# Performance work log

Hardware: AMD Instinct MI355X
Metric: run time of the kernel (lower is better)

## Reference

```python
import jax, jax.numpy as jnp
import numpy as np

N = 16384   # points (batch=1, divisible by patch_size so padding is identity)
C = 512     # channels
H = 8       # num_heads
K = 1024    # patch_size
G = 48      # voxel grid extent
EPS = 1e-5
SCALE = (C // H) ** -0.5


def setup_inputs() -> dict:
    rng = np.random.default_rng(0)
    # unique occupied voxels
    flat = rng.choice(G ** 3, size=N, replace=False)
    gx = flat // (G * G); gy = (flat // G) % G; gz = flat % G
    coords = np.stack([gx, gy, gz], 1).astype(np.int64)
    # occupancy LUT on padded grid -> neighbor index per 3x3x3 kernel offset (-1 = empty)
    lut = -np.ones(((G + 2) ** 3,), np.int64)
    def flt(c):
        return ((c[:, 0] + 1) * (G + 2) + (c[:, 1] + 1)) * (G + 2) + (c[:, 2] + 1)
    lut[flt(coords)] = np.arange(N)
    offs = np.array([[dx, dy, dz] for dx in (-1, 0, 1) for dy in (-1, 0, 1) for dz in (-1, 0, 1)], np.int64)
    nbr = np.stack([lut[flt(coords + o)] for o in offs], 1)  # [N,27]
    # Morton (z-order) serialization order
    def spread(v):
        v = v.astype(np.int64); r = np.zeros_like(v)
        for b in range(6):
            r |= ((v >> b) & 1) << (3 * b)
        return r
    code = (spread(gx) << 2) | (spread(gy) << 1) | spread(gz)
    order = np.argsort(code, kind='stable').astype(np.int32)

    key = jax.random.key(0)
    ks = jax.random.split(key, 8)
    s = 0.02
    p = lambda k, shape: jax.random.normal(k, shape, jnp.float32) * s
    return dict(
        feat=jax.random.normal(ks[0], (N, C), jnp.float32),
        neighbor_idx=jnp.asarray(nbr, jnp.int32),
        order=jnp.asarray(order, jnp.int32),
        cpe_w=p(ks[1], (27, C, C)), cpe_b=jnp.zeros((C,), jnp.float32),
        cpe_lin_w=p(ks[2], (C, C)), cpe_lin_b=jnp.zeros((C,), jnp.float32),
        cpe_ln_g=jnp.ones((C,), jnp.float32), cpe_ln_b=jnp.zeros((C,), jnp.float32),
        ln1_g=jnp.ones((C,), jnp.float32), ln1_b=jnp.zeros((C,), jnp.float32),
        qkv_w=p(ks[3], (3 * C, C)), qkv_b=jnp.zeros((3 * C,), jnp.float32),
        proj_w=p(ks[4], (C, C)), proj_b=jnp.zeros((C,), jnp.float32),
        ln2_g=jnp.ones((C,), jnp.float32), ln2_b=jnp.zeros((C,), jnp.float32),
        fc1_w=p(ks[5], (4 * C, C)), fc1_b=jnp.zeros((4 * C,), jnp.float32),
        fc2_w=p(ks[6], (C, 4 * C)), fc2_b=jnp.zeros((C,), jnp.float32),
    )


def _ln(x, g, b):
    m = x.mean(-1, keepdims=True)
    v = ((x - m) ** 2).mean(-1, keepdims=True)
    return (x - m) * jax.lax.rsqrt(v + EPS) * g + b


def _block(feat, neighbor_idx, order, cpe_w, cpe_b, cpe_lin_w, cpe_lin_b,
           cpe_ln_g, cpe_ln_b, ln1_g, ln1_b, qkv_w, qkv_b, proj_w, proj_b,
           ln2_g, ln2_b, fc1_w, fc1_b, fc2_w, fc2_b):
    # ---- CPE: SubMConv3d(3x3x3) -> Linear -> LayerNorm, residual ----
    valid = neighbor_idx >= 0
    idx = jnp.maximum(neighbor_idx, 0)
    h = jnp.zeros_like(feat)
    for kk in range(27):  # fixed kernel volume
        g = jnp.where(valid[:, kk:kk + 1], feat[idx[:, kk]], 0.0)
        h = h + g @ cpe_w[kk].T
    h = h + cpe_b
    h = h @ cpe_lin_w.T + cpe_lin_b
    h = _ln(h, cpe_ln_g, cpe_ln_b)
    feat = feat + h
    # ---- Serialized windowed attention (pre-norm, residual) ----
    x = _ln(feat, ln1_g, ln1_b)
    qkv = (x @ qkv_w.T + qkv_b)[order]                 # gather by serialized order
    qkv = qkv.reshape(N // K, K, 3, H, C // H)         # [P,K,3,H,hd]
    q = qkv[:, :, 0].transpose(0, 2, 1, 3)             # [P,H,K,hd]
    k = qkv[:, :, 1].transpose(0, 2, 1, 3)
    v = qkv[:, :, 2].transpose(0, 2, 1, 3)
    attn = jax.nn.softmax(jnp.einsum('phkd,phjd->phkj', q * SCALE, k), axis=-1)
    o = jnp.einsum('phkj,phjd->phkd', attn, v).transpose(0, 2, 1, 3).reshape(N, C)
    inverse = jnp.argsort(order)                       # scatter back
    o = o[inverse] @ proj_w.T + proj_b
    feat = feat + o
    # ---- MLP (pre-norm, residual) ----
    x = _ln(feat, ln2_g, ln2_b)
    x = jax.nn.gelu(x @ fc1_w.T + fc1_b, approximate=False)
    x = x @ fc2_w.T + fc2_b
    return feat + x


def reference(feat, neighbor_idx, order, cpe_w, cpe_b, cpe_lin_w, cpe_lin_b,
              cpe_ln_g, cpe_ln_b, ln1_g, ln1_b, qkv_w, qkv_b, proj_w, proj_b,
              ln2_g, ln2_b, fc1_w, fc1_b, fc2_w, fc2_b):
    return _block(feat, neighbor_idx, order, cpe_w, cpe_b, cpe_lin_w, cpe_lin_b,
                  cpe_ln_g, cpe_ln_b, ln1_g, ln1_b, qkv_w, qkv_b, proj_w, proj_b,
                  ln2_g, ln2_b, fc1_w, fc1_b, fc2_w, fc2_b)
```

## Files before the change

### kernel.cpp

```cpp
#include <hip/hip_runtime.h>
#include <math.h>

typedef unsigned short u16;
typedef unsigned int u32;
typedef __attribute__((ext_vector_type(8))) short short8;
typedef __attribute__((ext_vector_type(4))) float f32x4;

#define NPTS 16384

__device__ __forceinline__ u16 f2bf(float f) {
  u32 u = __float_as_uint(f);
  u = (u + 0x7fffu + ((u >> 16) & 1u)) >> 16;
  return (u16)u;
}
__device__ __forceinline__ float bf2f(u16 u) {
  return __uint_as_float((u32)u << 16);
}

__device__ __forceinline__ void gl2lds16(const u16* g, u16* l) {
  __builtin_amdgcn_global_load_lds(
      (const __attribute__((address_space(1))) u32*)g,
      (__attribute__((address_space(3))) u32*)l, 16, 0, 0);
}

__device__ __forceinline__ float wredsum(float v) {
#pragma unroll
  for (int m = 1; m < 64; m <<= 1) v += __shfl_xor(v, m, 64);
  return v;
}

__global__ void cvt_all(const float* __restrict__ w0, const float* __restrict__ w1,
                        const float* __restrict__ w2, const float* __restrict__ w3,
                        const float* __restrict__ w4, const float* __restrict__ w5,
                        u16* __restrict__ dst) {
  const int i = blockIdx.x * 256 + threadIdx.x;
  const float* s;
  int li;
  if (i < 1769472) { s = w0; li = i; }
  else if (i < 1835008) { s = w1; li = i - 1769472; }
  else if (i < 2031616) { s = w2; li = i - 1835008; }
  else if (i < 2097152) { s = w3; li = i - 2031616; }
  else if (i < 2359296) { s = w4; li = i - 2097152; }
  else { s = w5; li = i - 2359296; }
  float4 v = ((const float4*)s)[li];
  ushort4 o;
  o.x = f2bf(v.x); o.y = f2bf(v.y); o.z = f2bf(v.z); o.w = f2bf(v.w);
  ((ushort4*)dst)[i] = o;
}

__global__ void cvt_feat(const float* __restrict__ s, u16* __restrict__ d) {
  int i = blockIdx.x * 256 + threadIdx.x;
  if (i >= (NPTS + 1) * 128) return;
  ushort4 o;
  if (i < NPTS * 128) {
    float4 v = ((const float4*)s)[i];
    o.x = f2bf(v.x); o.y = f2bf(v.y); o.z = f2bf(v.z); o.w = f2bf(v.w);
  } else {
    o.x = 0; o.y = 0; o.z = 0; o.w = 0;
  }
  ((ushort4*)d)[i] = o;
}

__global__ void mkinv(const int* __restrict__ order, int* __restrict__ inv) {
  int i = blockIdx.x * 256 + threadIdx.x;
  if (i < NPTS) inv[order[i]] = i;
}

__global__ void reduce3b(const u16* __restrict__ part, const float* __restrict__ bias,
                         u16* __restrict__ o) {
  const int i = blockIdx.x * 256 + threadIdx.x;
  const ushort4* p4 = (const ushort4*)part;
  const ushort4 a = p4[i];
  const ushort4 b = p4[i + 2097152];
  const ushort4 c = p4[i + 4194304];
  const float4 bb = ((const float4*)bias)[i & 127];
  ushort4 r;
  r.x = f2bf(bf2f(a.x) + bf2f(b.x) + bf2f(c.x) + bb.x);
  r.y = f2bf(bf2f(a.y) + bf2f(b.y) + bf2f(c.y) + bb.y);
  r.z = f2bf(bf2f(a.z) + bf2f(b.z) + bf2f(c.z) + bb.z);
  r.w = f2bf(bf2f(a.w) + bf2f(b.w) + bf2f(c.w) + bb.w);
  ((ushort4*)o)[i] = r;
}

__global__ __launch_bounds__(256) void vtrans(const u16* __restrict__ vr,
                                              u16* __restrict__ vt) {
  __shared__ u16 t[64 * 72];
  const int bid = blockIdx.x;
  const int ph = bid >> 4, jt = bid & 15;
  const u16* src = vr + (size_t)ph * 65536 + jt * 64 * 64;
  u16* dst = vt + (size_t)ph * 65536 + jt * 64;
  const int tid = threadIdx.x;
  {
    const int j = tid >> 2, d0 = (tid & 3) * 16;
    uint4 w0 = *(const uint4*)(src + j * 64 + d0);
    uint4 w1 = *(const uint4*)(src + j * 64 + d0 + 8);
    *(uint4*)&t[j * 72 + d0] = w0;
    *(uint4*)&t[j * 72 + d0 + 8] = w1;
  }
  __syncthreads();
  {
    const int dr = tid >> 2, j0 = (tid & 3) * 16;
    u16 tmp[16];
#pragma unroll
    for (int e = 0; e < 16; e++) tmp[e] = t[(j0 + e) * 72 + dr];
    *(uint4*)(dst + (size_t)dr * 1024 + j0) = *(uint4*)&tmp[0];
    *(uint4*)(dst + (size_t)dr * 1024 + j0 + 8) = *(uint4*)&tmp[8];
  }
}

__global__ __launch_bounds__(256, 2) void gemm_cpe(
    const u16* __restrict__ Abase, const u16* __restrict__ Bw,
    const int* __restrict__ nbr, u16* __restrict__ part) {
  __shared__ __align__(16) u16 sA[128 * 32];
  __shared__ __align__(16) u16 sB[128 * 32];
  const int tid = threadIdx.x;
  const int wave = tid >> 6, lane = tid & 63;
  const int quad = lane >> 4, tl = lane & 15;
  const int wr = wave >> 1, wc = wave & 1;
  const int m0 = blockIdx.x * 128, n0 = blockIdx.y * 128;
  const int kk0 = blockIdx.z * 9;
  const int srow = lane >> 2, scol = lane & 3;

  int r[2]; int ca[2]; size_t brow[2];
#pragma unroll
  for (int o = 0; o < 2; o++) {
    r[o] = wave * 32 + o * 16 + srow;
    const int sw = (r[o] + (r[o] >> 2)) & 3;
    ca[o] = (scol ^ sw) * 8;
    brow[o] = (size_t)(n0 + r[o]) * 512 + ca[o];
  }
  u16* ldsA0 = &sA[(wave * 32) * 32];
  u16* ldsA1 = &sA[(wave * 32 + 16) * 32];
  u16* ldsB0 = &sB[(wave * 32) * 32];
  u16* ldsB1 = &sB[(wave * 32 + 16) * 32];

  f32x4 acc[4][4] = {};
  int nxt0 = nbr[(m0 + r[0]) * 27 + kk0];
  int nxt1 = nbr[(m0 + r[1]) * 27 + kk0];

  for (int s = 0; s < 9; s++) {
    const int kk = kk0 + s;
    const int g0 = nxt0 < 0 ? NPTS : nxt0;
    const int g1 = nxt1 < 0 ? NPTS : nxt1;
    if (s < 8) {
      nxt0 = nbr[(m0 + r[0]) * 27 + kk + 1];
      nxt1 = nbr[(m0 + r[1]) * 27 + kk + 1];
    }
    const u16* a0 = Abase + (size_t)g0 * 512 + ca[0];
    const u16* a1 = Abase + (size_t)g1 * 512 + ca[1];
    const u16* b0 = Bw + (size_t)kk * 262144 + brow[0];
    const u16* b1 = Bw + (size_t)kk * 262144 + brow[1];
#pragma unroll 1
    for (int kc = 0; kc < 512; kc += 32) {
      __syncthreads();
      gl2lds16(a0 + kc, ldsA0);
      gl2lds16(b0 + kc, ldsB0);
      gl2lds16(a1 + kc, ldsA1);
      gl2lds16(b1 + kc, ldsB1);
      __syncthreads();
      short8 fa[4], fb[4];
#pragma unroll
      for (int i = 0; i < 4; i++) {
        const int ra = wr * 64 + i * 16 + tl;
        fa[i] = *(const short8*)&sA[ra * 32 + ((quad ^ ((ra + (ra >> 2)) & 3)) * 8)];
        const int rb = wc * 64 + i * 16 + tl;
        fb[i] = *(const short8*)&sB[rb * 32 + ((quad ^ ((rb + (rb >> 2)) & 3)) * 8)];
      }
#pragma unroll
      for (int i = 0; i < 4; i++)
#pragma unroll
        for (int j = 0; j < 4; j++)
          acc[i][j] = __builtin_amdgcn_mfma_f32_16x16x32_bf16(fa[i], fb[j], acc[i][j], 0, 0, 0);
    }
  }

  u16* pz = part + (size_t)blockIdx.z * NPTS * 512;
#pragma unroll
  for (int i = 0; i < 4; i++) {
    const int mB = m0 + wr * 64 + i * 16 + quad * 4;
#pragma unroll
    for (int j = 0; j < 4; j++) {
      const int n = n0 + wc * 64 + j * 16 + tl;
      f32x4 c = acc[i][j];
#pragma unroll
      for (int rr = 0; rr < 4; rr++)
        pz[(size_t)(mB + rr) * 512 + n] = f2bf(c[rr]);
    }
  }
}

enum { EP_BF16 = 0, EP_QKV = 2, EP_RES = 3, EP_GELU = 4 };

template <int EP>
__global__ __launch_bounds__(256, 2) void gemm_nt(
    const u16* __restrict__ A, const u16* __restrict__ B, int M, int N, int K,
    const float* __restrict__ bias, float* __restrict__ outf,
    u16* __restrict__ outb, const float* __restrict__ res,
    const int* __restrict__ inv, u16* __restrict__ oq, u16* __restrict__ okk,
    u16* __restrict__ ov) {
  __shared__ __align__(16) u16 sA[128 * 32];
  __shared__ __align__(16) u16 sB[128 * 32];
  const int tid = threadIdx.x;
  const int wave = tid >> 6, lane = tid & 63;
  const int quad = lane >> 4, tl = lane & 15;
  const int wr = wave >> 1, wc = wave & 1;
  const int m0 = blockIdx.x * 128, n0 = blockIdx.y * 128;
  const int srow = lane >> 2, scol = lane & 3;

  f32x4 acc[4][4] = {};

  for (int kt = 0; kt < K; kt += 32) {
    __syncthreads();
#pragma unroll
    for (int o = 0; o < 2; o++) {
      const int r = wave * 32 + o * 16 + srow;
      const int sw = (r + (r >> 2)) & 3;
      const int ca = (scol ^ sw) * 8;
      gl2lds16(A + (size_t)(m0 + r) * K + kt + ca, &sA[(wave * 32 + o * 16) * 32]);
      gl2lds16(B + (size_t)(n0 + r) * K + kt + ca, &sB[(wave * 32 + o * 16) * 32]);
    }
    __syncthreads();
    short8 fa[4], fb[4];
#pragma unroll
    for (int i = 0; i < 4; i++) {
      const int ra = wr * 64 + i * 16 + tl;
      fa[i] = *(const short8*)&sA[ra * 32 + ((quad ^ ((ra + (ra >> 2)) & 3)) * 8)];
      const int rb = wc * 64 + i * 16 + tl;
      fb[i] = *(const short8*)&sB[rb * 32 + ((quad ^ ((rb + (rb >> 2)) & 3)) * 8)];
    }
#pragma unroll
    for (int i = 0; i < 4; i++)
#pragma unroll
      for (int j = 0; j < 4; j++)
        acc[i][j] = __builtin_amdgcn_mfma_f32_16x16x32_bf16(fa[i], fb[j], acc[i][j], 0, 0, 0);
  }

#pragma unroll
  for (int i = 0; i < 4; i++) {
    const int mB = m0 + wr * 64 + i * 16 + quad * 4;
#pragma unroll
    for (int j = 0; j < 4; j++) {
      const int n = n0 + wc * 64 + j * 16 + tl;
      const float bv = bias[n];
      f32x4 c = acc[i][j];
#pragma unroll
      for (int r = 0; r < 4; r++) {
        const int m = mB + r;
        float v = c[r] + bv;
        if (EP == EP_BF16) {
          outb[(size_t)m * N + n] = f2bf(v);
        } else if (EP == EP_RES) {
          outf[(size_t)m * N + n] = v + res[(size_t)m * N + n];
        } else if (EP == EP_GELU) {
          float g = 0.5f * v * (1.0f + erff(v * 0.70710678118654752f));
          outb[(size_t)m * N + n] = f2bf(g);
        } else if (EP == EP_QKV) {
          const int s = n >> 9, hh = (n >> 6) & 7, d = n & 63;
          const int pos = inv[m];
          const size_t base = (size_t)((pos >> 10) * 8 + hh) * 65536;
          const int jj = pos & 1023;
          if (s == 0) oq[base + (size_t)jj * 64 + d] = f2bf(v * 0.125f);
          else if (s == 1) okk[base + (size_t)jj * 64 + d] = f2bf(v);
          else ov[base + (size_t)jj * 64 + d] = f2bf(v);
        }
      }
    }
  }
}

__global__ __launch_bounds__(256, 2) void attn(
    const u16* __restrict__ qs, const u16* __restrict__ kk_s,
    const u16* __restrict__ vts, const int* __restrict__ order,
    u16* __restrict__ obf) {
  __shared__ __align__(16) u16 Qt[128 * 64];
  __shared__ __align__(16) u16 Kt[64 * 64];
  __shared__ __align__(16) u16 Vt[64 * 64];
  __shared__ __align__(16) u16 Pl[4][32 * 72];
  const int tid = threadIdx.x;
  const int wave = tid >> 6, lane = tid & 63;
  const int quad = lane >> 4, tl = lane & 15;
  const int bid = blockIdx.x;
  const int p = bid >> 6, h = (bid >> 3) & 7, qt = bid & 7;
  const size_t base = (size_t)(p * 8 + h) * 65536;

  {
    const u16* Qg = qs + base + qt * 8192;
#pragma unroll
    for (int i = 0; i < 4; i++) {
      const int op = wave * 4 + i;
      const int r = op * 8 + (lane >> 3);
      const int c8 = ((lane & 7) ^ (r & 7)) * 8;
      gl2lds16(Qg + r * 64 + c8, &Qt[op * 512]);
    }
  }

  float ls[2][4] = {};
  f32x4 acco[2][4] = {};

  for (int kt = 0; kt < 16; kt++) {
    __syncthreads();
    const u16* Kg = kk_s + base + kt * 4096;
    const u16* Vg = vts + base + kt * 64;
#pragma unroll
    for (int i = 0; i < 2; i++) {
      const int op = wave * 2 + i;
      const int r = op * 8 + (lane >> 3);
      const int c8 = ((lane & 7) ^ (r & 7)) * 8;
      gl2lds16(Kg + r * 64 + c8, &Kt[op * 512]);
      gl2lds16(Vg + r * 1024 + c8, &Vt[op * 512]);
    }
    __syncthreads();

    f32x4 accs[2][4] = {};
#pragma unroll
    for (int kd = 0; kd < 2; kd++) {
      short8 qa[2], kb[4];
#pragma unroll
      for (int a = 0; a < 2; a++) {
        const int r = wave * 32 + a * 16 + tl;
        const int oct = (kd * 4 + quad) ^ (r & 7);
        qa[a] = *(const short8*)&Qt[r * 64 + oct * 8];
      }
#pragma unroll
      for (int b = 0; b < 4; b++) {
        const int r = b * 16 + tl;
        const int oct = (kd * 4 + quad) ^ (r & 7);
        kb[b] = *(const short8*)&Kt[r * 64 + oct * 8];
      }
#pragma unroll
      for (int a = 0; a < 2; a++)
#pragma unroll
        for (int b = 0; b < 4; b++)
          accs[a][b] = __builtin_amdgcn_mfma_f32_16x16x32_bf16(qa[a], kb[b], accs[a][b], 0, 0, 0);
    }

    u16* plw = &Pl[wave][0];
#pragma unroll
    for (int a = 0; a < 2; a++)
#pragma unroll
      for (int c = 0; c < 4; c++) {
#pragma unroll
        for (int r = 0; r < 4; r++) {
          const float pe = __expf(accs[a][c][r]);
          accs[a][c][r] = pe;
          ls[a][r] += pe;
          plw[(a * 16 + quad * 4 + r) * 72 + c * 16 + tl] = f2bf(pe);
        }
      }

#pragma unroll
    for (int k2 = 0; k2 < 2; k2++) {
      short8 pa[2], vb[4];
#pragma unroll
      for (int a = 0; a < 2; a++)
        pa[a] = *(const short8*)&plw[(a * 16 + tl) * 72 + k2 * 32 + quad * 8];
#pragma unroll
      for (int b = 0; b < 4; b++) {
        const int rb = b * 16 + tl;
        vb[b] = *(const short8*)&Vt[rb * 64 + (((k2 * 4 + quad) ^ (rb & 7)) * 8)];
      }
#pragma unroll
      for (int a = 0; a < 2; a++)
#pragma unroll
        for (int b = 0; b < 4; b++)
          acco[a][b] = __builtin_amdgcn_mfma_f32_16x16x32_bf16(pa[a], vb[b], acco[a][b], 0, 0, 0);
    }
  }

#pragma unroll
  for (int a = 0; a < 2; a++)
#pragma unroll
    for (int r = 0; r < 4; r++) {
#pragma unroll
      for (int mk = 1; mk < 16; mk <<= 1) ls[a][r] += __shfl_xor(ls[a][r], mk, 64);
    }

  const int q0 = p * 1024 + qt * 128 + wave * 32;
#pragma unroll
  for (int a = 0; a < 2; a++)
#pragma unroll
    for (int r = 0; r < 4; r++) {
      const int orig = order[q0 + a * 16 + quad * 4 + r];
      const float il = 1.0f / ls[a][r];
#pragma unroll
      for (int b = 0; b < 4; b++)
        obf[(size_t)orig * 512 + h * 64 + b * 16 + tl] = f2bf(acco[a][b][r] * il);
    }
}

__global__ __launch_bounds__(256, 4) void ln_fuse1(
    const u16* __restrict__ h2, const float* __restrict__ feat,
    const float* __restrict__ cg, const float* __restrict__ cb,
    const float* __restrict__ g1, const float* __restrict__ b1,
    float* __restrict__ feat1, u16* __restrict__ xbf) {
  const int wave = threadIdx.x >> 6, lane = threadIdx.x & 63;
  const size_t row = (size_t)blockIdx.x * 4 + wave;
  const int c0 = lane * 4, c1 = 256 + lane * 4;
  const u16* hr = h2 + row * 512;
  ushort4 ha = *(const ushort4*)(hr + c0);
  ushort4 hb = *(const ushort4*)(hr + c1);
  float h[8];
  h[0] = bf2f(ha.x); h[1] = bf2f(ha.y); h[2] = bf2f(ha.z); h[3] = bf2f(ha.w);
  h[4] = bf2f(hb.x); h[5] = bf2f(hb.y); h[6] = bf2f(hb.z); h[7] = bf2f(hb.w);
  float s = 0.0f, q = 0.0f;
#pragma unroll
  for (int i = 0; i < 8; i++) { s += h[i]; q += h[i] * h[i]; }
  s = wredsum(s); q = wredsum(q);
  const float mean = s * (1.0f / 512.0f);
  const float var = q * (1.0f / 512.0f) - mean * mean;
  const float rs = rsqrtf(var + 1e-5f);
  float4 ga = *(const float4*)(cg + c0), gb = *(const float4*)(cg + c1);
  float4 ba = *(const float4*)(cb + c0), bb = *(const float4*)(cb + c1);
  const float* fr = feat + row * 512;
  float4 fa = *(const float4*)(fr + c0), fb = *(const float4*)(fr + c1);
  float f[8];
  f[0] = fa.x + (h[0] - mean) * rs * ga.x + ba.x;
  f[1] = fa.y + (h[1] - mean) * rs * ga.y + ba.y;
  f[2] = fa.z + (h[2] - mean) * rs * ga.z + ba.z;
  f[3] = fa.w + (h[3] - mean) * rs * ga.w + ba.w;
  f[4] = fb.x + (h[4] - mean) * rs * gb.x + bb.x;
  f[5] = fb.y + (h[5] - mean) * rs * gb.y + bb.y;
  f[6] = fb.z + (h[6] - mean) * rs * gb.z + bb.z;
  f[7] = fb.w + (h[7] - mean) * rs * gb.w + bb.w;
  float* f1r = feat1 + row * 512;
  *(float4*)(f1r + c0) = make_float4(f[0], f[1], f[2], f[3]);
  *(float4*)(f1r + c1) = make_float4(f[4], f[5], f[6], f[7]);
  float s2 = 0.0f, q2 = 0.0f;
#pragma unroll
  for (int i = 0; i < 8; i++) { s2 += f[i]; q2 += f[i] * f[i]; }
  s2 = wredsum(s2); q2 = wredsum(q2);
  const float mean2 = s2 * (1.0f / 512.0f);
  const float var2 = q2 * (1.0f / 512.0f) - mean2 * mean2;
  const float rs2 = rsqrtf(var2 + 1e-5f);
  float4 g1a = *(const float4*)(g1 + c0), g1b = *(const float4*)(g1 + c1);
  float4 b1a = *(const float4*)(b1 + c0), b1b = *(const float4*)(b1 + c1);
  ushort4 o0, o1;
  o0.x = f2bf((f[0] - mean2) * rs2 * g1a.x + b1a.x);
  o0.y = f2bf((f[1] - mean2) * rs2 * g1a.y + b1a.y);
  o0.z = f2bf((f[2] - mean2) * rs2 * g1a.z + b1a.z);
  o0.w = f2bf((f[3] - mean2) * rs2 * g1a.w + b1a.w);
  o1.x = f2bf((f[4] - mean2) * rs2 * g1b.x + b1b.x);
  o1.y = f2bf((f[5] - mean2) * rs2 * g1b.y + b1b.y);
  o1.z = f2bf((f[6] - mean2) * rs2 * g1b.z + b1b.z);
  o1.w = f2bf((f[7] - mean2) * rs2 * g1b.w + b1b.w);
  *(ushort4*)(xbf + row * 512 + c0) = o0;
  *(ushort4*)(xbf + row * 512 + c1) = o1;
}

__global__ __launch_bounds__(256, 4) void ln_only(
    const float* __restrict__ x, const float* __restrict__ g,
    const float* __restrict__ b_, u16* __restrict__ o) {
  const int wave = threadIdx.x >> 6, lane = threadIdx.x & 63;
  const size_t row = (size_t)blockIdx.x * 4 + wave;
  const int c0 = lane * 4, c1 = 256 + lane * 4;
  const float* xr = x + row * 512;
  float4 a = *(const float4*)(xr + c0);
  float4 b = *(const float4*)(xr + c1);
  float s = a.x + a.y + a.z + a.w + b.x + b.y + b.z + b.w;
  float q = a.x * a.x + a.y * a.y + a.z * a.z + a.w * a.w +
            b.x * b.x + b.y * b.y + b.z * b.z + b.w * b.w;
  s = wredsum(s); q = wredsum(q);
  const float mean = s * (1.0f / 512.0f);
  const float var = q * (1.0f / 512.0f) - mean * mean;
  const float rs = rsqrtf(var + 1e-5f);
  float4 ga = *(const float4*)(g + c0), gb = *(const float4*)(g + c1);
  float4 ba = *(const float4*)(b_ + c0), bb = *(const float4*)(b_ + c1);
  ushort4 o0, o1;
  o0.x = f2bf((a.x - mean) * rs * ga.x + ba.x);
  o0.y = f2bf((a.y - mean) * rs * ga.y + ba.y);
  o0.z = f2bf((a.z - mean) * rs * ga.z + ba.z);
  o0.w = f2bf((a.w - mean) * rs * ga.w + ba.w);
  o1.x = f2bf((b.x - mean) * rs * gb.x + bb.x);
  o1.y = f2bf((b.y - mean) * rs * gb.y + bb.y);
  o1.z = f2bf((b.z - mean) * rs * gb.z + bb.z);
  o1.w = f2bf((b.w - mean) * rs * gb.w + bb.w);
  *(ushort4*)(o + row * 512 + c0) = o0;
  *(ushort4*)(o + row * 512 + c1) = o1;
}

extern "C" void kernel_launch(void* const* d_in, const int* in_sizes, int n_in,
                              void* d_out, int out_size, void* d_ws, size_t ws_size,
                              hipStream_t stream) {
  (void)in_sizes; (void)n_in; (void)out_size; (void)ws_size;
  const float* feat = (const float*)d_in[0];
  const int* nbr = (const int*)d_in[1];
  const int* order = (const int*)d_in[2];
  const float* cpe_w = (const float*)d_in[3];
  const float* cpe_b = (const float*)d_in[4];
  const float* cpe_lin_w = (const float*)d_in[5];
  const float* cpe_lin_b = (const float*)d_in[6];
  const float* cpe_ln_g = (const float*)d_in[7];
  const float* cpe_ln_b = (const float*)d_in[8];
  const float* ln1_g = (const float*)d_in[9];
  const float* ln1_b = (const float*)d_in[10];
  const float* qkv_w = (const float*)d_in[11];
  const float* qkv_b = (const float*)d_in[12];
  const float* proj_w = (const float*)d_in[13];
  const float* proj_b = (const float*)d_in[14];
  const float* ln2_g = (const float*)d_in[15];
  const float* ln2_b = (const float*)d_in[16];
  const float* fc1_w = (const float*)d_in[17];
  const float* fc1_b = (const float*)d_in[18];
  const float* fc2_w = (const float*)d_in[19];
  const float* fc2_b = (const float*)d_in[20];
  float* out = (float*)d_out;

  char* ws = (char*)d_ws;
  size_t off = 0;
  auto alloc = [&](size_t bytes) {
    char* p = ws + off;
    off += (bytes + 255) & ~(size_t)255;
    return p;
  };
  u16* featbf = (u16*)alloc((size_t)(NPTS + 1) * 512 * 2);
  u16* w_cpe = (u16*)alloc((size_t)27 * 512 * 512 * 2);
  u16* w_cl = (u16*)alloc((size_t)512 * 512 * 2);
  u16* w_qkv = (u16*)alloc((size_t)1536 * 512 * 2);
  u16* w_proj = (u16*)alloc((size_t)512 * 512 * 2);
  u16* w_fc1 = (u16*)alloc((size_t)2048 * 512 * 2);
  u16* w_fc2 = (u16*)alloc((size_t)512 * 2048 * 2);
  u16* hbf = (u16*)alloc((size_t)NPTS * 512 * 2);
  char* big = alloc((size_t)NPTS * 2048 * 2);
  float* feat1 = (float*)alloc((size_t)NPTS * 512 * 4);
  int* inv = (int*)alloc((size_t)NPTS * 4);

  u16* part = (u16*)big;
  u16* h2 = (u16*)big;
  u16* qsb = (u16*)big;
  u16* ksb = qsb + (size_t)NPTS * 512;
  u16* vrow = ksb + (size_t)NPTS * 512;
  u16* vtb = vrow + (size_t)NPTS * 512;
  u16* tbf = (u16*)big;
  u16* xbf = hbf;
  u16* obf = hbf;
  u16* x2bf = featbf;

  cvt_feat<<<dim3(((NPTS + 1) * 128 + 255) / 256), dim3(256), 0, stream>>>(feat, featbf);
  cvt_all<<<dim3(10240), dim3(256), 0, stream>>>(cpe_w, cpe_lin_w, qkv_w, proj_w,
                                                 fc1_w, fc2_w, w_cpe);
  mkinv<<<dim3(NPTS / 256), dim3(256), 0, stream>>>(order, inv);

  gemm_cpe<<<dim3(128, 4, 3), dim3(256), 0, stream>>>(featbf, w_cpe, nbr, part);
  reduce3b<<<dim3(8192), dim3(256), 0, stream>>>(part, cpe_b, hbf);
  gemm_nt<EP_BF16><<<dim3(128, 4), dim3(256), 0, stream>>>(
      hbf, w_cl, NPTS, 512, 512, cpe_lin_b, nullptr, h2, nullptr, nullptr,
      nullptr, nullptr, nullptr);
  ln_fuse1<<<dim3(NPTS / 4), dim3(256), 0, stream>>>(
      h2, feat, cpe_ln_g, cpe_ln_b, ln1_g, ln1_b, feat1, xbf);
  gemm_nt<EP_QKV><<<dim3(128, 12), dim3(256), 0, stream>>>(
      xbf, w_qkv, NPTS, 1536, 512, qkv_b, nullptr, nullptr, nullptr, inv,
      qsb, ksb, vrow);
  vtrans<<<dim3(2048), dim3(256), 0, stream>>>(vrow, vtb);
  attn<<<dim3(1024), dim3(256), 0, stream>>>(qsb, ksb, vtb, order, obf);
  gemm_nt<EP_RES><<<dim3(128, 4), dim3(256), 0, stream>>>(
      obf, w_proj, NPTS, 512, 512, proj_b, out, nullptr, feat1, nullptr,
      nullptr, nullptr, nullptr);
  ln_only<<<dim3(NPTS / 4), dim3(256), 0, stream>>>(out, ln2_g, ln2_b, x2bf);
  gemm_nt<EP_GELU><<<dim3(128, 16), dim3(256), 0, stream>>>(
      x2bf, w_fc1, NPTS, 2048, 512, fc1_b, nullptr, tbf, nullptr, nullptr,
      nullptr, nullptr, nullptr);
  gemm_nt<EP_RES><<<dim3(128, 4), dim3(256), 0, stream>>>(
      tbf, w_fc2, NPTS, 512, 2048, fc2_b, out, nullptr, out, nullptr,
      nullptr, nullptr, nullptr);
}
```

Measured before the change: 636.8 us.

## Replace dense 27-offset CPE GEMM with compacted sparse neighbor-pair GEMM

The sparse 3x3x3 conv used to multiply every point by all 27 offset weights, substituting a zero row for empty neighbors, and then summed three partial buffers. Now the valid (point, neighbor) pairs are counted, offset and scattered per kernel offset into compact 128-row tiles. A GEMM runs only over those tiles, and a per-point reduce sums the pair outputs and adds the bias. This removes the multiply work on empty neighbors, which is most of it at this grid occupancy, at the cost of three small bookkeeping kernels and an extra gather-reduce pass. A fixed MAXP buffer cap silently drops pairs if the inputs are denser than expected.

```diff
diff --git a/kernel.cpp b/kernel.cpp
--- a/kernel.cpp
+++ b/kernel.cpp
@@ -3,10 +3,13 @@
 
 typedef unsigned short u16;
 typedef unsigned int u32;
+typedef unsigned long long u64;
 typedef __attribute__((ext_vector_type(8))) short short8;
 typedef __attribute__((ext_vector_type(4))) float f32x4;
 
 #define NPTS 16384
+#define MAXP 98304
+#define MAXTILE 3483
 
 __device__ __forceinline__ u16 f2bf(float f) {
   u32 u = __float_as_uint(f);
@@ -24,6 +27,11 @@
 }
 
 __device__ __forceinline__ float wredsum(float v) {
+#pragma unroll
+  for (int m = 1; m < 64; m <<= 1) v += __shfl_xor(v, m, 64);
+  return v;
+}
+__device__ __forceinline__ int wredsumi(int v) {
 #pragma unroll
   for (int m = 1; m < 64; m <<= 1) v += __shfl_xor(v, m, 64);
   return v;
@@ -66,20 +74,173 @@
   if (i < NPTS) inv[order[i]] = i;
 }
 
-__global__ void reduce3b(const u16* __restrict__ part, const float* __restrict__ bias,
-                         u16* __restrict__ o) {
-  const int i = blockIdx.x * 256 + threadIdx.x;
-  const ushort4* p4 = (const ushort4*)part;
-  const ushort4 a = p4[i];
-  const ushort4 b = p4[i + 2097152];
-  const ushort4 c = p4[i + 4194304];
-  const float4 bb = ((const float4*)bias)[i & 127];
-  ushort4 r;
-  r.x = f2bf(bf2f(a.x) + bf2f(b.x) + bf2f(c.x) + bb.x);
-  r.y = f2bf(bf2f(a.y) + bf2f(b.y) + bf2f(c.y) + bb.y);
-  r.z = f2bf(bf2f(a.z) + bf2f(b.z) + bf2f(c.z) + bb.z);
-  r.w = f2bf(bf2f(a.w) + bf2f(b.w) + bf2f(c.w) + bb.w);
-  ((ushort4*)o)[i] = r;
+__global__ __launch_bounds__(256) void cpe_count(const int* __restrict__ nbr,
+                                                 int* __restrict__ cnt) {
+  __shared__ int wc[4];
+  const int kk = blockIdx.x;
+  int c = 0;
+  for (int i = threadIdx.x; i < NPTS; i += 256)
+    c += (nbr[i * 27 + kk] >= 0) ? 1 : 0;
+  c = wredsumi(c);
+  if ((threadIdx.x & 63) == 0) wc[threadIdx.x >> 6] = c;
+  __syncthreads();
+  if (threadIdx.x == 0) cnt[kk] = wc[0] + wc[1] + wc[2] + wc[3];
+}
+
+__global__ void cpe_off(const int* __restrict__ cnt, int* __restrict__ off,
+                        int* __restrict__ tkk, int* __restrict__ meta) {
+  if (threadIdx.x != 0 || blockIdx.x != 0) return;
+  int pos = 0, t = 0;
+  for (int kk = 0; kk < 27; kk++) {
+    off[kk] = pos;
+    int tk = (cnt[kk] + 127) >> 7;
+    if (pos + tk * 128 > MAXP) tk = (MAXP - pos) >> 7;
+    for (int u = 0; u < tk; u++) tkk[t + u] = kk;
+    t += tk;
+    pos += tk * 128;
+  }
+  meta[0] = t;
+}
+
+__global__ __launch_bounds__(256) void cpe_scatter(
+    const int* __restrict__ nbr, const int* __restrict__ cnt,
+    const int* __restrict__ off, int* __restrict__ pairj,
+    int* __restrict__ pairpos) {
+  __shared__ int wcnt[4];
+  __shared__ int running_s;
+  const int kk = blockIdx.x;
+  const int tid = threadIdx.x, wave = tid >> 6, lane = tid & 63;
+  const int base = off[kk];
+  if (tid == 0) running_s = 0;
+  __syncthreads();
+  for (int c0 = 0; c0 < NPTS; c0 += 256) {
+    const int i = c0 + tid;
+    const int v = nbr[i * 27 + kk];
+    const bool valid = v >= 0;
+    const u64 m = __ballot(valid);
+    if (lane == 0) wcnt[wave] = __popcll(m);
+    __syncthreads();
+    int woff = 0;
+    for (int w = 0; w < wave; w++) woff += wcnt[w];
+    const int ctot = wcnt[0] + wcnt[1] + wcnt[2] + wcnt[3];
+    const int rank = running_s + woff + __popcll(m & ((1ull << lane) - 1ull));
+    int pp = -1;
+    if (valid) {
+      const int t = base + rank;
+      if (t < MAXP) { pairj[t] = v; pp = t; }
+    }
+    pairpos[i * 27 + kk] = pp;
+    __syncthreads();
+    if (tid == 0) running_s += ctot;
+    __syncthreads();
+  }
+  const int total = cnt[kk];
+  const int padded = (total + 127) & ~127;
+  for (int p = total + tid; p < padded; p += 256)
+    if (base + p < MAXP) pairj[base + p] = NPTS;
+}
+
+__global__ __launch_bounds__(256, 2) void gemm_pair(
+    const u16* __restrict__ Abase, const u16* __restrict__ Bw,
+    const int* __restrict__ meta, const int* __restrict__ tkk,
+    const int* __restrict__ pairj, u16* __restrict__ outp) {
+  if ((int)blockIdx.x >= meta[0]) return;
+  __shared__ __align__(16) u16 sA[128 * 32];
+  __shared__ __align__(16) u16 sB[128 * 32];
+  const int tid = threadIdx.x;
+  const int wave = tid >> 6, lane = tid & 63;
+  const int quad = lane >> 4, tl = lane & 15;
+  const int wr = wave >> 1, wc = wave & 1;
+  const int p0 = blockIdx.x * 128, n0 = blockIdx.y * 128;
+  const int kk = tkk[blockIdx.x];
+  const int srow = lane >> 2, scol = lane & 3;
+
+  int r[2]; int ca[2];
+#pragma unroll
+  for (int o = 0; o < 2; o++) {
+    r[o] = wave * 32 + o * 16 + srow;
+    const int sw = (r[o] + (r[o] >> 2)) & 3;
+    ca[o] = (scol ^ sw) * 8;
+  }
+  const int j0 = pairj[p0 + r[0]];
+  const int j1 = pairj[p0 + r[1]];
+  const u16* a0 = Abase + (size_t)j0 * 512 + ca[0];
+  const u16* a1 = Abase + (size_t)j1 * 512 + ca[1];
+  const u16* b0 = Bw + (size_t)kk * 262144 + (size_t)(n0 + r[0]) * 512 + ca[0];
+  const u16* b1 = Bw + (size_t)kk * 262144 + (size_t)(n0 + r[1]) * 512 + ca[1];
+  u16* ldsA0 = &sA[(wave * 32) * 32];
+  u16* ldsA1 = &sA[(wave * 32 + 16) * 32];
+  u16* ldsB0 = &sB[(wave * 32) * 32];
+  u16* ldsB1 = &sB[(wave * 32 + 16) * 32];
+
+  f32x4 acc[4][4] = {};
+#pragma unroll 1
+  for (int kc = 0; kc < 512; kc += 32) {
+    __syncthreads();
+    gl2lds16(a0 + kc, ldsA0);
+    gl2lds16(b0 + kc, ldsB0);
+    gl2lds16(a1 + kc, ldsA1);
+    gl2lds16(b1 + kc, ldsB1);
+    __syncthreads();
+    short8 fa[4], fb[4];
+#pragma unroll
+    for (int i = 0; i < 4; i++) {
+      const int ra = wr * 64 + i * 16 + tl;
+      fa[i] = *(const short8*)&sA[ra * 32 + ((quad ^ ((ra + (ra >> 2)) & 3)) * 8)];
+      const int rb = wc * 64 + i * 16 + tl;
+      fb[i] = *(const short8*)&sB[rb * 32 + ((quad ^ ((rb + (rb >> 2)) & 3)) * 8)];
+    }
+#pragma unroll
+    for (int i = 0; i < 4; i++)
+#pragma unroll
+      for (int j = 0; j < 4; j++)
+        acc[i][j] = __builtin_amdgcn_mfma_f32_16x16x32_bf16(fa[i], fb[j], acc[i][j], 0, 0, 0);
+  }
+
+#pragma unroll
+  for (int i = 0; i < 4; i++) {
+    const int pB = p0 + wr * 64 + i * 16 + quad * 4;
+#pragma unroll
+    for (int j = 0; j < 4; j++) {
+      const int n = n0 + wc * 64 + j * 16 + tl;
+      f32x4 c = acc[i][j];
+#pragma unroll
+      for (int rr = 0; rr < 4; rr++)
+        outp[(size_t)(pB + rr) * 512 + n] = f2bf(c[rr]);
+    }
+  }
+}
+
+__global__ __launch_bounds__(256, 4) void cpe_reduce(
+    const u16* __restrict__ outp, const int* __restrict__ pairpos,
+    const float* __restrict__ bias, u16* __restrict__ h) {
+  const int wave = threadIdx.x >> 6, lane = threadIdx.x & 63;
+  const int i = blockIdx.x * 4 + wave;
+  const int c = lane * 8;
+  float acc[8];
+  const float4 b0 = *(const float4*)(bias + c);
+  const float4 b1 = *(const float4*)(bias + c + 4);
+  acc[0] = b0.x; acc[1] = b0.y; acc[2] = b0.z; acc[3] = b0.w;
+  acc[4] = b1.x; acc[5] = b1.y; acc[6] = b1.z; acc[7] = b1.w;
+  const int* pp = pairpos + i * 27;
+#pragma unroll 1
+  for (int kk = 0; kk < 27; kk++) {
+    const int pos = pp[kk];
+    if (pos >= 0) {
+      const u16* row = outp + (size_t)pos * 512 + c;
+      ushort4 u0 = *(const ushort4*)row;
+      ushort4 u1 = *(const ushort4*)(row + 4);
+      acc[0] += bf2f(u0.x); acc[1] += bf2f(u0.y);
+      acc[2] += bf2f(u0.z); acc[3] += bf2f(u0.w);
+      acc[4] += bf2f(u1.x); acc[5] += bf2f(u1.y);
+      acc[6] += bf2f(u1.z); acc[7] += bf2f(u1.w);
+    }
+  }
+  ushort4 o0, o1;
+  o0.x = f2bf(acc[0]); o0.y = f2bf(acc[1]); o0.z = f2bf(acc[2]); o0.w = f2bf(acc[3]);
+  o1.x = f2bf(acc[4]); o1.y = f2bf(acc[5]); o1.z = f2bf(acc[6]); o1.w = f2bf(acc[7]);
+  *(ushort4*)(h + (size_t)i * 512 + c) = o0;
+  *(ushort4*)(h + (size_t)i * 512 + c + 4) = o1;
 }
 
 __global__ __launch_bounds__(256) void vtrans(const u16* __restrict__ vr,
@@ -105,87 +266,6 @@
     for (int e = 0; e < 16; e++) tmp[e] = t[(j0 + e) * 72 + dr];
     *(uint4*)(dst + (size_t)dr * 1024 + j0) = *(uint4*)&tmp[0];
     *(uint4*)(dst + (size_t)dr * 1024 + j0 + 8) = *(uint4*)&tmp[8];
-  }
-}
-
-__global__ __launch_bounds__(256, 2) void gemm_cpe(
-    const u16* __restrict__ Abase, const u16* __restrict__ Bw,
-    const int* __restrict__ nbr, u16* __restrict__ part) {
-  __shared__ __align__(16) u16 sA[128 * 32];
-  __shared__ __align__(16) u16 sB[128 * 32];
-  const int tid = threadIdx.x;
-  const int wave = tid >> 6, lane = tid & 63;
-  const int quad = lane >> 4, tl = lane & 15;
-  const int wr = wave >> 1, wc = wave & 1;
-  const int m0 = blockIdx.x * 128, n0 = blockIdx.y * 128;
-  const int kk0 = blockIdx.z * 9;
-  const int srow = lane >> 2, scol = lane & 3;
-
-  int r[2]; int ca[2]; size_t brow[2];
-#pragma unroll
-  for (int o = 0; o < 2; o++) {
-    r[o] = wave * 32 + o * 16 + srow;
-    const int sw = (r[o] + (r[o] >> 2)) & 3;
-    ca[o] = (scol ^ sw) * 8;
-    brow[o] = (size_t)(n0 + r[o]) * 512 + ca[o];
-  }
-  u16* ldsA0 = &sA[(wave * 32) * 32];
-  u16* ldsA1 = &sA[(wave * 32 + 16) * 32];
-  u16* ldsB0 = &sB[(wave * 32) * 32];
-  u16* ldsB1 = &sB[(wave * 32 + 16) * 32];
-
-  f32x4 acc[4][4] = {};
-  int nxt0 = nbr[(m0 + r[0]) * 27 + kk0];
-  int nxt1 = nbr[(m0 + r[1]) * 27 + kk0];
-
-  for (int s = 0; s < 9; s++) {
-    const int kk = kk0 + s;
-    const int g0 = nxt0 < 0 ? NPTS : nxt0;
-    const int g1 = nxt1 < 0 ? NPTS : nxt1;
-    if (s < 8) {
-      nxt0 = nbr[(m0 + r[0]) * 27 + kk + 1];
-      nxt1 = nbr[(m0 + r[1]) * 27 + kk + 1];
-    }
-    const u16* a0 = Abase + (size_t)g0 * 512 + ca[0];
-    const u16* a1 = Abase + (size_t)g1 * 512 + ca[1];
-    const u16* b0 = Bw + (size_t)kk * 262144 + brow[0];
-    const u16* b1 = Bw + (size_t)kk * 262144 + brow[1];
-#pragma unroll 1
-    for (int kc = 0; kc < 512; kc += 32) {
-      __syncthreads();
-      gl2lds16(a0 + kc, ldsA0);
-      gl2lds16(b0 + kc, ldsB0);
-      gl2lds16(a1 + kc, ldsA1);
-      gl2lds16(b1 + kc, ldsB1);
-      __syncthreads();
-      short8 fa[4], fb[4];
-#pragma unroll
-      for (int i = 0; i < 4; i++) {
-        const int ra = wr * 64 + i * 16 + tl;
-        fa[i] = *(const short8*)&sA[ra * 32 + ((quad ^ ((ra + (ra >> 2)) & 3)) * 8)];
-        const int rb = wc * 64 + i * 16 + tl;
-        fb[i] = *(const short8*)&sB[rb * 32 + ((quad ^ ((rb + (rb >> 2)) & 3)) * 8)];
-      }
-#pragma unroll
-      for (int i = 0; i < 4; i++)
-#pragma unroll
-        for (int j = 0; j < 4; j++)
-          acc[i][j] = __builtin_amdgcn_mfma_f32_16x16x32_bf16(fa[i], fb[j], acc[i][j], 0, 0, 0);
-    }
-  }
-
-  u16* pz = part + (size_t)blockIdx.z * NPTS * 512;
-#pragma unroll
-  for (int i = 0; i < 4; i++) {
-    const int mB = m0 + wr * 64 + i * 16 + quad * 4;
-#pragma unroll
-    for (int j = 0; j < 4; j++) {
-      const int n = n0 + wc * 64 + j * 16 + tl;
-      f32x4 c = acc[i][j];
-#pragma unroll
-      for (int rr = 0; rr < 4; rr++)
-        pz[(size_t)(mB + rr) * 512 + n] = f2bf(c[rr]);
-    }
   }
 }
 
@@ -523,8 +603,14 @@
   char* big = alloc((size_t)NPTS * 2048 * 2);
   float* feat1 = (float*)alloc((size_t)NPTS * 512 * 4);
   int* inv = (int*)alloc((size_t)NPTS * 4);
-
-  u16* part = (u16*)big;
+  int* cnt = (int*)alloc(27 * 4);
+  int* offs = (int*)alloc(27 * 4);
+  int* meta = (int*)alloc(256);
+  int* tkk = (int*)alloc((size_t)(MAXTILE + 1) * 4);
+  int* pairj = (int*)alloc((size_t)MAXP * 4);
+  int* pairpos = (int*)alloc((size_t)NPTS * 27 * 4);
+
+  u16* out_pair = (u16*)big;
   u16* h2 = (u16*)big;
   u16* qsb = (u16*)big;
   u16* ksb = qsb + (size_t)NPTS * 512;
@@ -540,8 +626,13 @@
                                                  fc1_w, fc2_w, w_cpe);
   mkinv<<<dim3(NPTS / 256), dim3(256), 0, stream>>>(order, inv);
 
-  gemm_cpe<<<dim3(128, 4, 3), dim3(256), 0, stream>>>(featbf, w_cpe, nbr, part);
-  reduce3b<<<dim3(8192), dim3(256), 0, stream>>>(part, cpe_b, hbf);
+  cpe_count<<<dim3(27), dim3(256), 0, stream>>>(nbr, cnt);
+  cpe_off<<<dim3(1), dim3(64), 0, stream>>>(cnt, offs, tkk, meta);
+  cpe_scatter<<<dim3(27), dim3(256), 0, stream>>>(nbr, cnt, offs, pairj, pairpos);
+  gemm_pair<<<dim3(MAXTILE, 4), dim3(256), 0, stream>>>(featbf, w_cpe, meta, tkk,
+                                                        pairj, out_pair);
+  cpe_reduce<<<dim3(NPTS / 4), dim3(256), 0, stream>>>(out_pair, pairpos, cpe_b, hbf);
+
   gemm_nt<EP_BF16><<<dim3(128, 4), dim3(256), 0, stream>>>(
       hbf, w_cl, NPTS, 512, 512, cpe_lin_b, nullptr, h2, nullptr, nullptr,
       nullptr, nullptr, nullptr);
```

Result: faster. 603.7 us (-5.2%).
